# Kernel tuning notes

Measured on AMD Instinct MI355X. Metric: run time of the kernel, lower is better.

Reference implementation:

```python
import jax, jax.numpy as jnp
import numpy as np

UP = (2, 2)            # zero-insertion upsampling factors (H, W)
DOWN = (1, 1)          # downsampling strides
PAD = ((2, 1), (2, 1)) # same-padding from _calc_padding for k=4, up=2, down=1
GAIN = 1.0             # module gain; CUDA path multiplies by prod(up)


def setup_inputs() -> dict:
    key = jax.random.key(0)
    x = jax.random.normal(key, (16, 64, 128, 128), dtype=jnp.float32)
    # _setup_kernel: 1D [1,3,3,1] -> outer product (separable=False since numel<8),
    # normalized by abs-sum (=64); flip_kernel=False, gain**(ndim/rank)=1.
    k1d = jnp.array([1.0, 3.0, 3.0, 1.0], dtype=jnp.float32)
    kernel = jnp.outer(k1d, k1d)
    kernel = kernel / jnp.sum(jnp.abs(kernel))
    return {"x": x, "kernel": kernel}


def _upfirdn2d(x, kernel):
    # Fused zero-insert upsample + FIR conv + downsample, expressed as a single
    # depthwise dilated convolution (lhs_dilation does the zero insertion,
    # window_strides does the downsampling) -- no large intermediates.
    C = x.shape[1]
    # flip_kernel=False => true convolution; lax does correlation, so flip here.
    k = kernel[::-1, ::-1]
    w = jnp.tile(k[None, None].astype(x.dtype), (C, 1, 1, 1))  # [C,1,kh,kw]
    out = jax.lax.conv_general_dilated(
        x, w,
        window_strides=DOWN,
        padding=PAD,
        lhs_dilation=UP,
        dimension_numbers=("NCHW", "OIHW", "NCHW"),
        feature_group_count=C,
    )
    return out * (GAIN * UP[0] * UP[1])  # gain *= prod(up) as in CUDA path


def reference(x, kernel):
    # output: [16, 64, 256, 256]
    return _upfirdn2d(x, kernel)
```

## Files before the change

### kernel.cpp

```cpp
#include <hip/hip_runtime.h>


#define IN_H 128
#define IN_W 128
#define OUT_H 255
#define OUT_W 255
#define ROWS_PER_TILE 16
#define NTILES 16
#define LDS_STRIDE 130
#define MAX_IN_ROWS 10

__global__ __launch_bounds__(256) void upfirdn2d_kernel(
    const float* __restrict__ x,
    const float* __restrict__ k,
    float* __restrict__ out)
{
    __shared__ float lw[16];
    __shared__ float li[MAX_IN_ROWS * LDS_STRIDE];

    const int tid   = threadIdx.x;
    const int tile  = blockIdx.x;
    const int plane = blockIdx.y;

    const int oy0       = tile * ROWS_PER_TILE;
    const int nrows_out = min(ROWS_PER_TILE, OUT_H - oy0);
    const int iy_lo     = (oy0 >> 1) - 1;
    const int iy_hi     = min(IN_H - 1, (oy0 >> 1) + 8);
    const int n_in_rows = iy_hi - iy_lo + 1;

    if (tid < 16) {
        const int py = (tid >> 3) & 1;
        const int px = (tid >> 2) & 1;
        const int a  = (tid >> 1) & 1;
        const int b  = tid & 1;
        const int ry = py ? (a ? 0 : 2) : (a ? 1 : 3);
        const int rx = px ? (b ? 0 : 2) : (b ? 1 : 3);
        lw[(((py << 1) | px) << 2) + ((a << 1) | b)] = 4.0f * k[ry * 4 + rx];
    }

    {
        const float4* xp4 = (const float4*)(x + (size_t)plane * (IN_H * IN_W));
        const int nslots = n_in_rows * (IN_W / 4);
        for (int s = tid; s < nslots; s += 256) {
            const int row = s >> 5;
            const int c4  = s & 31;
            const int iy  = iy_lo + row;
            float4 v = make_float4(0.f, 0.f, 0.f, 0.f);
            if (iy >= 0) v = xp4[iy * (IN_W / 4) + c4];
            float* dst = &li[row * LDS_STRIDE + 1 + (c4 << 2)];
            dst[0] = v.x; dst[1] = v.y; dst[2] = v.z; dst[3] = v.w;
        }
        if (tid < MAX_IN_ROWS) li[tid * LDS_STRIDE] = 0.0f;
    }
    __syncthreads();

    auto compute = [&](int oy, int ox) -> float {
        const int py = oy & 1, px = ox & 1;
        const int r  = ((oy >> 1) - 1 + py) - iy_lo;
        const int c  = (ox >> 1) + px;
        const float4 w = *(const float4*)&lw[(((py << 1) | px) << 2)];
        const float* p0 = &li[r * LDS_STRIDE + c];
        const float* p1 = p0 + LDS_STRIDE;
        return w.x * p0[0] + w.y * p0[1] + w.z * p1[0] + w.w * p1[1];
    };

    const int out_base = plane * (OUT_H * OUT_W) + oy0 * OUT_W;
    const int n_out    = nrows_out * OUT_W;
    const int end_i    = out_base + n_out;
    const int astart   = (out_base + 3) & ~3;
    const int aend     = end_i & ~3;
    const int head_n   = astart - out_base;
    const int tail_n   = end_i - aend;

    if (tid < head_n) {
        out[out_base + tid] = compute(oy0, tid);
    }
    if (tid < tail_n) {
        const unsigned rel = (unsigned)(aend + tid - out_base);
        const unsigned q   = rel / 255u;
        out[aend + tid] = compute(oy0 + (int)q, (int)(rel - q * 255u));
    }

    const int ngroups = (aend - astart) >> 2;
    for (int g = tid; g < ngroups; g += 256) {
        const int f0 = astart + (g << 2);
        const unsigned rel = (unsigned)(f0 - out_base);
        const unsigned q   = rel / 255u;
        int ox = (int)(rel - q * 255u);
        int oy = oy0 + (int)q;
        float4 res;
        float* rp = &res.x;
#pragma unroll
        for (int j = 0; j < 4; ++j) {
            rp[j] = compute(oy, ox);
            if (++ox == OUT_W) { ox = 0; ++oy; }
        }
        *(float4*)(out + f0) = res;
    }
}

extern "C" void kernel_launch(void* const* d_in, const int* in_sizes, int n_in,
                              void* d_out, int out_size, void* d_ws, size_t ws_size,
                              hipStream_t stream) {
    const float* x = (const float*)d_in[0];
    const float* k = (const float*)d_in[1];
    float* out = (float*)d_out;

    dim3 block(256, 1, 1);
    dim3 grid(NTILES, 1024, 1);
    upfirdn2d_kernel<<<grid, block, 0, stream>>>(x, k, out);
}
```

Baseline: 356.7 us.

## Map threads to output columns with a register sliding window over input rows

Each thread now owns one output column and walks down the tile's rows, keeping the two current input rows in registers and loading only one new row pair per step. This removes the per-element divide by 255 and the head/tail alignment handling, and reuses shared-memory reads across vertically adjacent outputs. The shared-memory staging switches to aligned float4 stores by padding the stride to 132. In exchange, global stores become scalar (still coalesced across the wave) instead of float4, and one thread per block sits idle.

```diff
diff --git a/kernel.cpp b/kernel.cpp
--- a/kernel.cpp
+++ b/kernel.cpp
@@ -7,7 +7,7 @@
 #define OUT_W 255
 #define ROWS_PER_TILE 16
 #define NTILES 16
-#define LDS_STRIDE 130
+#define LDS_STRIDE 132
 #define MAX_IN_ROWS 10
 
 __global__ __launch_bounds__(256) void upfirdn2d_kernel(
@@ -47,55 +47,42 @@
             const int iy  = iy_lo + row;
             float4 v = make_float4(0.f, 0.f, 0.f, 0.f);
             if (iy >= 0) v = xp4[iy * (IN_W / 4) + c4];
-            float* dst = &li[row * LDS_STRIDE + 1 + (c4 << 2)];
-            dst[0] = v.x; dst[1] = v.y; dst[2] = v.z; dst[3] = v.w;
+            *(float4*)&li[row * LDS_STRIDE + 4 + (c4 << 2)] = v;
         }
-        if (tid < MAX_IN_ROWS) li[tid * LDS_STRIDE] = 0.0f;
+        if (tid < MAX_IN_ROWS) li[tid * LDS_STRIDE + 3] = 0.0f;
     }
     __syncthreads();
 
-    auto compute = [&](int oy, int ox) -> float {
-        const int py = oy & 1, px = ox & 1;
-        const int r  = ((oy >> 1) - 1 + py) - iy_lo;
-        const int c  = (ox >> 1) + px;
-        const float4 w = *(const float4*)&lw[(((py << 1) | px) << 2)];
-        const float* p0 = &li[r * LDS_STRIDE + c];
-        const float* p1 = p0 + LDS_STRIDE;
-        return w.x * p0[0] + w.y * p0[1] + w.z * p1[0] + w.w * p1[1];
-    };
+    if (tid >= OUT_W) return;
 
-    const int out_base = plane * (OUT_H * OUT_W) + oy0 * OUT_W;
-    const int n_out    = nrows_out * OUT_W;
-    const int end_i    = out_base + n_out;
-    const int astart   = (out_base + 3) & ~3;
-    const int aend     = end_i & ~3;
-    const int head_n   = astart - out_base;
-    const int tail_n   = end_i - aend;
+    const int px = tid & 1;
+    const float4 we = *(const float4*)&lw[px << 2];
+    const float4 wo = *(const float4*)&lw[(2 | px) << 2];
+    const int col0 = 3 + (tid >> 1) + px;
 
-    if (tid < head_n) {
-        out[out_base + tid] = compute(oy0, tid);
-    }
-    if (tid < tail_n) {
-        const unsigned rel = (unsigned)(aend + tid - out_base);
-        const unsigned q   = rel / 255u;
-        out[aend + tid] = compute(oy0 + (int)q, (int)(rel - q * 255u));
-    }
+    const float* l0 = &li[col0];
+    float a0 = l0[0],           a1 = l0[1];
+    float b0 = l0[LDS_STRIDE],  b1 = l0[LDS_STRIDE + 1];
 
-    const int ngroups = (aend - astart) >> 2;
-    for (int g = tid; g < ngroups; g += 256) {
-        const int f0 = astart + (g << 2);
-        const unsigned rel = (unsigned)(f0 - out_base);
-        const unsigned q   = rel / 255u;
-        int ox = (int)(rel - q * 255u);
-        int oy = oy0 + (int)q;
-        float4 res;
-        float* rp = &res.x;
+    float* op = out + (size_t)plane * (OUT_H * OUT_W) + oy0 * OUT_W + tid;
+
 #pragma unroll
-        for (int j = 0; j < 4; ++j) {
-            rp[j] = compute(oy, ox);
-            if (++ox == OUT_W) { ox = 0; ++oy; }
+    for (int j = 0; j < 8; ++j) {
+        op[0] = we.x * a0 + we.y * a1 + we.z * b0 + we.w * b1;
+
+        float c0 = 0.f, c1 = 0.f;
+        const int r2 = j + 2;
+        if (r2 < n_in_rows) {
+            const float* lr = &li[r2 * LDS_STRIDE + col0];
+            c0 = lr[0]; c1 = lr[1];
         }
-        *(float4*)(out + f0) = res;
+
+        if (2 * j + 1 < nrows_out) {
+            op[OUT_W] = wo.x * b0 + wo.y * b1 + wo.z * c0 + wo.w * c1;
+        }
+
+        a0 = b0; a1 = b1; b0 = c0; b1 = c1;
+        op += 2 * OUT_W;
     }
 }
 
```

Result: faster. 314.5 us (-11.8%).
